# Optimization experiments

Measured on AMD Instinct MI355X. Metric: run time of the kernel, lower is better.

## Reference

```python
import jax, jax.numpy as jnp
import numpy as np

N_UNARY = 16  # unary predicate count; joined width = 2*N_UNARY + 4 = 36

# Clauses parsed from KENN strings: (literal column indices, literal signs).
# Negated literal ('n' prefix) -> sign -1, positive -> +1.
UNARY_CLAUSES = [
    ([0, 1], [-1, 1]),
    ([1, 2], [-1, 1]),
    ([2, 3, 4], [-1, 1, 1]),
    ([4, 5], [-1, 1]),
    ([6, 7, 8], [-1, 1, 1]),
    ([8, 9], [-1, 1]),
    ([10, 11, 12], [-1, 1, 1]),
    ([13, 14, 15], [-1, 1, 1]),
]
# Joined-matrix columns: [0:16]=unary(x), [16:32]=unary(y), [32:36]=binary.
BINARY_CLAUSES = [
    ([0, 32, 16], [-1, -1, 1]),
    ([1, 33, 17], [-1, -1, 1]),
    ([2, 34, 18], [-1, -1, 1]),
    ([3, 35, 19], [-1, -1, 1]),
]


def _enhance(x, clauses, weights):
    """KnowledgeEnhancer: sum over ClauseEnhancer deltas.

    Per clause: gather literal columns, flip negated literals, softmax over
    literals (t-conorm boost), scale by clause weight, flip signs back, and
    scatter-add into the full predicate width.
    """
    delta = jnp.zeros_like(x)
    for i, (idx, sgn) in enumerate(clauses):
        idx_a = jnp.asarray(idx)
        sgn_a = jnp.asarray(sgn, x.dtype)
        sel = x[:, idx_a] * sgn_a                      # [N, k] signed literal preactivations
        contrib = weights[i] * sgn_a * jax.nn.softmax(sel, axis=1)
        delta = delta.at[:, idx_a].add(contrib)
    return delta


def setup_inputs() -> dict:
    key = jax.random.key(0)
    k1, k2, k3, k4 = jax.random.split(key, 4)
    n_nodes, n_edges = 100000, 2000000
    unary = jax.random.normal(k1, (n_nodes, N_UNARY), dtype=jnp.float32)
    binary = jax.random.normal(k2, (n_edges, 4), dtype=jnp.float32)
    index1 = jax.random.randint(k3, (n_edges,), 0, n_nodes)
    index2 = jax.random.randint(k4, (n_edges,), 0, n_nodes)
    # learnable clause weights ('_' weights), initial_clause_weight = 0.5
    unary_weights = jnp.full((len(UNARY_CLAUSES),), 0.5, dtype=jnp.float32)
    binary_weights = jnp.full((len(BINARY_CLAUSES),), 0.5, dtype=jnp.float32)
    return {
        "unary": unary,
        "binary": binary,
        "index1": index1,
        "index2": index2,
        "unary_weights": unary_weights,
        "binary_weights": binary_weights,
    }


def reference(unary, binary, index1, index2, unary_weights, binary_weights):
    # unary knowledge enhancement (residual)
    u = unary + _enhance(unary, UNARY_CLAUSES, unary_weights)
    # Join: gather endpoint unary rows, concat with binary -> [E, 2*n_unary + n_binary]
    joined = jnp.concatenate([u[index1], u[index2], binary], axis=1)
    # binary knowledge enhancement on the joined matrix
    deltas = _enhance(joined, BINARY_CLAUSES, binary_weights)
    # GroupBy: split deltas and scatter-reduce unary parts back to nodes
    du1 = deltas[:, :N_UNARY]
    du2 = deltas[:, N_UNARY:2 * N_UNARY]
    db = deltas[:, 2 * N_UNARY:]
    up = u.at[index1].add(du1).at[index2].add(du2)
    bp = binary + db
    # activation = identity (default lambda x: x)
    return up, bp
```

## Files before the change

kernel.cpp:

```cpp
#include <hip/hip_runtime.h>
#include <hip/hip_bf16.h>


#define NRANGE 13
#define RBITS  13
#define RSIZE  8192
#define NSLICE 16
#define EPB    1024
#define SEGCAP 1024
#define FXP_SCALE 2048.0f
#define FXP_INV   (1.0f / 2048.0f)

__device__ __forceinline__ void sm2(float xi, float xj, float w,
                                    float& di, float& dj) {
    float na = -xi, b = xj;
    float m  = fmaxf(na, b);
    float e0 = __expf(na - m), e1 = __expf(b - m);
    float inv = w / (e0 + e1);
    di -= e0 * inv;
    dj += e1 * inv;
}

__device__ __forceinline__ void sm3(float xi, float xj, float xk, float w,
                                    float& di, float& dj, float& dk) {
    float na = -xi, b = xj, c = xk;
    float m  = fmaxf(fmaxf(na, b), c);
    float e0 = __expf(na - m), e1 = __expf(b - m), e2 = __expf(c - m);
    float inv = w / (e0 + e1 + e2);
    di -= e0 * inv;
    dj += e1 * inv;
    dk += e2 * inv;
}

__global__ void unary_kernel(const float* __restrict__ x_in,
                             const float* __restrict__ uw,
                             float* __restrict__ up,
                             float4* __restrict__ u4,
                             int n_nodes) {
    int n = blockIdx.x * blockDim.x + threadIdx.x;
    if (n >= n_nodes) return;

    const float4* xr = (const float4*)(x_in + (size_t)n * 16);
    float4 r0 = xr[0], r1 = xr[1], r2 = xr[2], r3 = xr[3];
    float x[16] = {r0.x, r0.y, r0.z, r0.w,
                   r1.x, r1.y, r1.z, r1.w,
                   r2.x, r2.y, r2.z, r2.w,
                   r3.x, r3.y, r3.z, r3.w};
    float d[16];
#pragma unroll
    for (int i = 0; i < 16; ++i) d[i] = 0.0f;

    sm2(x[0],  x[1],          uw[0], d[0],  d[1]);
    sm2(x[1],  x[2],          uw[1], d[1],  d[2]);
    sm3(x[2],  x[3],  x[4],   uw[2], d[2],  d[3],  d[4]);
    sm2(x[4],  x[5],          uw[3], d[4],  d[5]);
    sm3(x[6],  x[7],  x[8],   uw[4], d[6],  d[7],  d[8]);
    sm2(x[8],  x[9],          uw[5], d[8],  d[9]);
    sm3(x[10], x[11], x[12],  uw[6], d[10], d[11], d[12]);
    sm3(x[13], x[14], x[15],  uw[7], d[13], d[14], d[15]);

    float4* w_up = (float4*)(up + (size_t)n * 16);
    float4 v0 = make_float4(x[0] + d[0], x[1] + d[1], x[2] + d[2], x[3] + d[3]);
    w_up[0] = v0;
#pragma unroll
    for (int i = 1; i < 4; ++i)
        w_up[i] = make_float4(x[4*i]   + d[4*i],   x[4*i+1] + d[4*i+1],
                              x[4*i+2] + d[4*i+2], x[4*i+3] + d[4*i+3]);
    u4[n] = v0;
}


__global__ __launch_bounds__(512)
void edge_compute_kernel(const float4* __restrict__ u4,
                         const float4* __restrict__ binary,
                         const int* __restrict__ idx1,
                         const int* __restrict__ idx2,
                         const float* __restrict__ bw,
                         unsigned long long* __restrict__ recs,
                         unsigned* __restrict__ cnts,
                         unsigned* __restrict__ offs,
                         float4* __restrict__ bp,
                         int n_edges) {
    __shared__ unsigned cnt[2][NRANGE];
    __shared__ unsigned off[2][NRANGE];
    int tid = threadIdx.x;
    if (tid < 2 * NRANGE) ((unsigned*)cnt)[tid] = 0;
    __syncthreads();

    float w[4] = {bw[0], bw[1], bw[2], bw[3]};

    int e[2]; bool valid[2];
    int i1[2], i2[2], r1[2], r2[2];
    unsigned rank1[2], rank2[2];
    unsigned long long q1[2], q2[2];
    float4 b4[2], a4[2], c4[2], dbv4[2];

#pragma unroll
    for (int k = 0; k < 2; ++k) {
        e[k] = blockIdx.x * EPB + k * 512 + tid;
        valid[k] = e[k] < n_edges;
        int ec = valid[k] ? e[k] : 0;
        i1[k] = idx1[ec];
        i2[k] = idx2[ec];
    }
#pragma unroll
    for (int k = 0; k < 2; ++k) {
        a4[k] = u4[i1[k]];
        c4[k] = u4[i2[k]];
        b4[k] = binary[valid[k] ? e[k] : 0];
    }

#pragma unroll
    for (int k = 0; k < 2; ++k) {
        float a[4]  = {a4[k].x, a4[k].y, a4[k].z, a4[k].w};
        float bb[4] = {b4[k].x, b4[k].y, b4[k].z, b4[k].w};
        float c[4]  = {c4[k].x, c4[k].y, c4[k].z, c4[k].w};
        unsigned p1[4], p2[4];
        float dbv[4];
#pragma unroll
        for (int i = 0; i < 4; ++i) {
            float na = -a[i], nb = -bb[i], cc = c[i];
            float m  = fmaxf(fmaxf(na, nb), cc);
            float e0 = __expf(na - m), e1 = __expf(nb - m), e2 = __expf(cc - m);
            float inv = w[i] / (e0 + e1 + e2);
            p1[i]  = __float2uint_rn(e0 * inv * FXP_SCALE);
            p2[i]  = __float2uint_rn(e2 * inv * FXP_SCALE);
            dbv[i] = bb[i] - e1 * inv;
        }
        q1[k] = (unsigned long long)(unsigned)(i1[k] & (RSIZE - 1))
              | ((unsigned long long)p1[0] << 13) | ((unsigned long long)p1[1] << 25)
              | ((unsigned long long)p1[2] << 37) | ((unsigned long long)p1[3] << 49);
        q2[k] = (unsigned long long)(unsigned)(i2[k] & (RSIZE - 1))
              | ((unsigned long long)p2[0] << 13) | ((unsigned long long)p2[1] << 25)
              | ((unsigned long long)p2[2] << 37) | ((unsigned long long)p2[3] << 49);
        dbv4[k] = make_float4(dbv[0], dbv[1], dbv[2], dbv[3]);
        r1[k] = i1[k] >> RBITS;
        r2[k] = i2[k] >> RBITS;
        if (valid[k]) {
            rank1[k] = atomicAdd(&cnt[0][r1[k]], 1u);
            rank2[k] = atomicAdd(&cnt[1][r2[k]], 1u);
        }
    }
    __syncthreads();
    if (tid < 2) {
        unsigned acc = 0;
#pragma unroll
        for (int r = 0; r < NRANGE; ++r) { off[tid][r] = acc; acc += cnt[tid][r]; }
    }
    __syncthreads();
    if (tid < 2 * NRANGE) {
        cnts[(size_t)blockIdx.x * 2 * NRANGE + tid] = ((unsigned*)cnt)[tid];
        offs[(size_t)blockIdx.x * 2 * NRANGE + tid] = ((unsigned*)off)[tid];
    }
    size_t segN = (size_t)blockIdx.x * 2 * SEGCAP;
#pragma unroll
    for (int k = 0; k < 2; ++k) {
        if (!valid[k]) continue;
        recs[segN          + off[0][r1[k]] + rank1[k]] = q1[k];
        recs[segN + SEGCAP + off[1][r2[k]] + rank2[k]] = q2[k];
        bp[e[k]] = dbv4[k];
    }
}

__global__ __launch_bounds__(1024)
void bin_kernel(const unsigned long long* __restrict__ recs,
                const unsigned* __restrict__ cnts,
                const unsigned* __restrict__ offs,
                unsigned long long* __restrict__ partials,
                int nblk) {
    __shared__ unsigned long long table[RSIZE];
    unsigned b    = blockIdx.x;
    unsigned s    = b % NSLICE;
    unsigned rr   = (b / NSLICE) % NRANGE;
    unsigned side = b / (NSLICE * NRANGE);

    for (int i = threadIdx.x; i < RSIZE; i += 1024) table[i] = 0ull;
    __syncthreads();

    unsigned bpg = ((unsigned)nblk + NSLICE - 1) / NSLICE;
    unsigned b0 = s * bpg;
    unsigned b1 = b0 + bpg;
    if (b1 > (unsigned)nblk) b1 = (unsigned)nblk;

    unsigned wid  = threadIdx.x >> 6;
    unsigned lane = threadIdx.x & 63;
    unsigned eb = b0 + wid;
    unsigned c_cur = 0, o_cur = 0;
    if (eb < b1) {
        unsigned base = (eb * 2u + side) * NRANGE + rr;
        c_cur = cnts[base];
        o_cur = offs[base];
    }
    while (eb < b1) {
        unsigned eb_n = eb + 16;
        unsigned c_n = 0, o_n = 0;
        if (eb_n < b1) {
            unsigned base_n = (eb_n * 2u + side) * NRANGE + rr;
            c_n = cnts[base_n];
            o_n = offs[base_n];
        }
        const unsigned long long* seg =
            recs + ((size_t)eb * 2 + side) * SEGCAP + o_cur;
        unsigned i = lane;
        for (; i + 64 < c_cur; i += 128) {
            unsigned long long ra = seg[i];
            unsigned long long rb = seg[i + 64];
            unsigned long long va =  ((ra >> 13) & 0xFFFull)
                                  | (((ra >> 25) & 0xFFFull) << 16)
                                  | (((ra >> 37) & 0xFFFull) << 32)
                                  | (((ra >> 49) & 0xFFFull) << 48);
            unsigned long long vb =  ((rb >> 13) & 0xFFFull)
                                  | (((rb >> 25) & 0xFFFull) << 16)
                                  | (((rb >> 37) & 0xFFFull) << 32)
                                  | (((rb >> 49) & 0xFFFull) << 48);
            atomicAdd(&table[(unsigned)ra & (RSIZE - 1)], va);
            atomicAdd(&table[(unsigned)rb & (RSIZE - 1)], vb);
        }
        if (i < c_cur) {
            unsigned long long ra = seg[i];
            unsigned long long va =  ((ra >> 13) & 0xFFFull)
                                  | (((ra >> 25) & 0xFFFull) << 16)
                                  | (((ra >> 37) & 0xFFFull) << 32)
                                  | (((ra >> 49) & 0xFFFull) << 48);
            atomicAdd(&table[(unsigned)ra & (RSIZE - 1)], va);
        }
        eb = eb_n;
        c_cur = c_n;
        o_cur = o_n;
    }
    __syncthreads();

    unsigned long long* dst = partials + (size_t)b * RSIZE;
    for (int i2 = threadIdx.x; i2 < RSIZE; i2 += 1024) dst[i2] = table[i2];
}

__global__ void merge_bin_kernel(const unsigned long long* __restrict__ partials,
                                 float* __restrict__ up, int n_nodes) {
    int n = blockIdx.x * blockDim.x + threadIdx.x;
    if (n >= n_nodes) return;
    unsigned rr = (unsigned)n >> RBITS;
    unsigned i  = (unsigned)n & (RSIZE - 1);

    const unsigned long long* pn =
        partials + ((size_t)(0 * NRANGE + rr) * NSLICE) * RSIZE + i;
    const unsigned long long* pp =
        partials + ((size_t)(1 * NRANGE + rr) * NSLICE) * RSIZE + i;
    unsigned long long qn = 0, qp = 0;
#pragma unroll
    for (int sl = 0; sl < NSLICE; ++sl) {
        qn += pn[(size_t)sl * RSIZE];
        qp += pp[(size_t)sl * RSIZE];
    }

    float4* dst = (float4*)(up + (size_t)n * 16);
    float4 cur = dst[0];
    float d0 = ((float)(unsigned)( qp        & 0xFFFF) -
                (float)(unsigned)( qn        & 0xFFFF)) * FXP_INV;
    float d1 = ((float)(unsigned)((qp >> 16) & 0xFFFF) -
                (float)(unsigned)((qn >> 16) & 0xFFFF)) * FXP_INV;
    float d2 = ((float)(unsigned)((qp >> 32) & 0xFFFF) -
                (float)(unsigned)((qn >> 32) & 0xFFFF)) * FXP_INV;
    float d3 = ((float)(unsigned)((qp >> 48) & 0xFFFF) -
                (float)(unsigned)((qn >> 48) & 0xFFFF)) * FXP_INV;
    dst[0] = make_float4(cur.x + d0, cur.y + d1, cur.z + d2, cur.w + d3);
}


__global__ void edge_atomic_kernel(const float* __restrict__ u,
                                   const float4* __restrict__ binary,
                                   const int* __restrict__ idx1,
                                   const int* __restrict__ idx2,
                                   const float* __restrict__ bw,
                                   unsigned long long* __restrict__ neg,
                                   unsigned long long* __restrict__ pos,
                                   float4* __restrict__ bp,
                                   int n_edges) {
    int e = blockIdx.x * blockDim.x + threadIdx.x;
    if (e >= n_edges) return;
    int n1 = idx1[e], n2 = idx2[e];
    float4 b4 = binary[e];
    float4 a4 = *(const float4*)(u + (size_t)n1 * 16);
    float4 c4 = *(const float4*)(u + (size_t)n2 * 16);
    float a[4]  = {a4.x, a4.y, a4.z, a4.w};
    float bb[4] = {b4.x, b4.y, b4.z, b4.w};
    float c[4]  = {c4.x, c4.y, c4.z, c4.w};
    unsigned long long q1 = 0, q2 = 0;
    float dbv[4];
#pragma unroll
    for (int i = 0; i < 4; ++i) {
        float na = -a[i], nb = -bb[i], cc = c[i];
        float m  = fmaxf(fmaxf(na, nb), cc);
        float e0 = __expf(na - m), e1 = __expf(nb - m), e2 = __expf(cc - m);
        float inv = bw[i] / (e0 + e1 + e2);
        q1 |= (unsigned long long)__float2uint_rn(e0 * inv * FXP_SCALE) << (16 * i);
        q2 |= (unsigned long long)__float2uint_rn(e2 * inv * FXP_SCALE) << (16 * i);
        dbv[i] = bb[i] - e1 * inv;
    }
    atomicAdd(&neg[n1], q1);
    atomicAdd(&pos[n2], q2);
    bp[e] = make_float4(dbv[0], dbv[1], dbv[2], dbv[3]);
}

__global__ void merge_atomic_kernel(const unsigned long long* __restrict__ neg,
                                    const unsigned long long* __restrict__ pos,
                                    float* __restrict__ up, int n_nodes) {
    int n = blockIdx.x * blockDim.x + threadIdx.x;
    if (n >= n_nodes) return;
    unsigned long long qn = neg[n], qp = pos[n];
    float4* dst = (float4*)(up + (size_t)n * 16);
    float4 cur = dst[0];
    float d0 = ((float)(unsigned)( qp        & 0xFFFF) -
                (float)(unsigned)( qn        & 0xFFFF)) * FXP_INV;
    float d1 = ((float)(unsigned)((qp >> 16) & 0xFFFF) -
                (float)(unsigned)((qn >> 16) & 0xFFFF)) * FXP_INV;
    float d2 = ((float)(unsigned)((qp >> 32) & 0xFFFF) -
                (float)(unsigned)((qn >> 32) & 0xFFFF)) * FXP_INV;
    float d3 = ((float)(unsigned)((qp >> 48) & 0xFFFF) -
                (float)(unsigned)((qn >> 48) & 0xFFFF)) * FXP_INV;
    dst[0] = make_float4(cur.x + d0, cur.y + d1, cur.z + d2, cur.w + d3);
}

extern "C" void kernel_launch(void* const* d_in, const int* in_sizes, int n_in,
                              void* d_out, int out_size, void* d_ws, size_t ws_size,
                              hipStream_t stream) {
    const float* unary   = (const float*)d_in[0];
    const float* binary  = (const float*)d_in[1];
    const int*   index1  = (const int*)d_in[2];
    const int*   index2  = (const int*)d_in[3];
    const float* uw      = (const float*)d_in[4];
    const float* bw      = (const float*)d_in[5];

    int n_nodes = in_sizes[0] / 16;
    int n_edges = in_sizes[2];

    float* out = (float*)d_out;
    float* up  = out;
    float* bp  = out + (size_t)n_nodes * 16;

    int nblk = (n_edges + EPB - 1) / EPB;

    size_t rec_bytes  = (size_t)nblk * 2 * SEGCAP * 8;
    size_t part_bytes = (size_t)2 * NRANGE * NSLICE * RSIZE * 8;
    size_t u4_bytes   = (size_t)n_nodes * 16;
    size_t cnt_bytes  = (size_t)nblk * 2 * NRANGE * 4;
    size_t need = rec_bytes + part_bytes + u4_bytes + 2 * cnt_bytes + 256;

    if (ws_size >= need) {
        char* w = (char*)d_ws;
        unsigned long long* recs     = (unsigned long long*)w;
        unsigned long long* partials = (unsigned long long*)(w + rec_bytes);
        float4*   u4   = (float4*)(w + rec_bytes + part_bytes);
        unsigned* cnts = (unsigned*)(w + rec_bytes + part_bytes + u4_bytes);
        unsigned* offs = cnts + (size_t)nblk * 2 * NRANGE;

        unary_kernel<<<(n_nodes + 255) / 256, 256, 0, stream>>>(
            unary, uw, up, u4, n_nodes);
        edge_compute_kernel<<<nblk, 512, 0, stream>>>(
            u4, (const float4*)binary, index1, index2, bw,
            recs, cnts, offs, (float4*)bp, n_edges);
        bin_kernel<<<2 * NRANGE * NSLICE, 1024, 0, stream>>>(
            recs, cnts, offs, partials, nblk);
        merge_bin_kernel<<<(n_nodes + 255) / 256, 256, 0, stream>>>(
            partials, up, n_nodes);
    } else {
        unsigned long long* neg = (unsigned long long*)d_ws;
        unsigned long long* pos = neg + n_nodes;
        float4* u4 = (float4*)(pos + n_nodes);
        hipMemsetAsync(neg, 0, (size_t)2 * n_nodes * 8, stream);
        unary_kernel<<<(n_nodes + 255) / 256, 256, 0, stream>>>(
            unary, uw, up, u4, n_nodes);
        edge_atomic_kernel<<<(n_edges + 255) / 256, 256, 0, stream>>>(
            up, (const float4*)binary, index1, index2, bw,
            neg, pos, (float4*)bp, n_edges);
        merge_atomic_kernel<<<(n_nodes + 255) / 256, 256, 0, stream>>>(
            neg, pos, up, n_nodes);
    }
}
```

Before: 168.4 us.

## Fuse four-stage binning pipeline into one persistent cooperative kernel with grid syncs

Replaces the four separate launches (unary, edge compute, bin, merge) with a single persistent cooperative kernel that runs each phase in a grid-stride loop and separates them with grid.sync. Edge records are first staged in LDS and then written out coalesced instead of scattered to global memory, and the binary output uses nontemporal stores. Chunk size doubles to 2048 edges per block. This targets launch overhead and scattered writes, but the grid is limited to about two blocks per CU, so the bin phase's 416 work items and the edge phase run with less parallelism. It also adds grid-wide barrier costs and host-side occupancy queries on every call.

New measurement: 599.7 us. +256.2%, slower.

```diff
diff --git a/kernel.cpp b/kernel.cpp
--- a/kernel.cpp
+++ b/kernel.cpp
@@ -1,15 +1,23 @@
 #include <hip/hip_runtime.h>
-#include <hip/hip_bf16.h>
+#include <hip/hip_cooperative_groups.h>
+
+namespace cg = cooperative_groups;
 
 
 #define NRANGE 13
 #define RBITS  13
 #define RSIZE  8192
 #define NSLICE 16
-#define EPB    1024
-#define SEGCAP 1024
+#define EPB    2048
 #define FXP_SCALE 2048.0f
 #define FXP_INV   (1.0f / 2048.0f)
+
+typedef float nf4 __attribute__((ext_vector_type(4)));
+
+__device__ __forceinline__ void nt_store_f4(float4 v, float4* p) {
+    nf4 t; t.x = v.x; t.y = v.y; t.z = v.z; t.w = v.w;
+    __builtin_nontemporal_store(t, (nf4*)p);
+}
 
 __device__ __forceinline__ void sm2(float xi, float xj, float w,
                                     float& di, float& dj) {
@@ -32,6 +40,247 @@
     dk += e2 * inv;
 }
 
+
+__global__ __launch_bounds__(1024, 8)
+void fused_kernel(const float* __restrict__ x_in,
+                  const float4* __restrict__ binary,
+                  const int* __restrict__ idx1,
+                  const int* __restrict__ idx2,
+                  const float* __restrict__ uw,
+                  const float* __restrict__ bw,
+                  float* __restrict__ up,
+                  float4* __restrict__ bp,
+                  float4* __restrict__ u4,
+                  unsigned long long* __restrict__ recs,
+                  unsigned* __restrict__ cnts,
+                  unsigned* __restrict__ offs,
+                  unsigned long long* __restrict__ partials,
+                  int n_nodes, int n_edges, int nchunk) {
+    __shared__ union SH {
+        struct {
+            unsigned cnt[2][NRANGE];
+            unsigned off[2][NRANGE];
+            unsigned long long stage[2][EPB];
+        } e;
+        unsigned long long table[RSIZE];
+    } sh;
+
+    cg::grid_group grid = cg::this_grid();
+    const int tid     = threadIdx.x;
+    const int nthread = gridDim.x * 1024;
+
+    for (int n = blockIdx.x * 1024 + tid; n < n_nodes; n += nthread) {
+        const float4* xr = (const float4*)(x_in + (size_t)n * 16);
+        float4 r0 = xr[0], r1 = xr[1], r2 = xr[2], r3 = xr[3];
+        float x[16] = {r0.x, r0.y, r0.z, r0.w, r1.x, r1.y, r1.z, r1.w,
+                       r2.x, r2.y, r2.z, r2.w, r3.x, r3.y, r3.z, r3.w};
+        float d[16];
+#pragma unroll
+        for (int i = 0; i < 16; ++i) d[i] = 0.0f;
+        sm2(x[0],  x[1],          uw[0], d[0],  d[1]);
+        sm2(x[1],  x[2],          uw[1], d[1],  d[2]);
+        sm3(x[2],  x[3],  x[4],   uw[2], d[2],  d[3],  d[4]);
+        sm2(x[4],  x[5],          uw[3], d[4],  d[5]);
+        sm3(x[6],  x[7],  x[8],   uw[4], d[6],  d[7],  d[8]);
+        sm2(x[8],  x[9],          uw[5], d[8],  d[9]);
+        sm3(x[10], x[11], x[12],  uw[6], d[10], d[11], d[12]);
+        sm3(x[13], x[14], x[15],  uw[7], d[13], d[14], d[15]);
+        float4* w_up = (float4*)(up + (size_t)n * 16);
+        float4 v0 = make_float4(x[0]+d[0], x[1]+d[1], x[2]+d[2], x[3]+d[3]);
+        w_up[0] = v0;
+#pragma unroll
+        for (int i = 1; i < 4; ++i)
+            w_up[i] = make_float4(x[4*i]+d[4*i],     x[4*i+1]+d[4*i+1],
+                                  x[4*i+2]+d[4*i+2], x[4*i+3]+d[4*i+3]);
+        u4[n] = v0;
+    }
+    __threadfence();
+    grid.sync();
+
+    {
+        float w[4] = {bw[0], bw[1], bw[2], bw[3]};
+        for (int chunk = blockIdx.x; chunk < nchunk; chunk += gridDim.x) {
+            if (tid < 2 * NRANGE) ((unsigned*)sh.e.cnt)[tid] = 0;
+            __syncthreads();
+
+            int e[2]; bool valid[2];
+            int i1[2], i2[2], r1[2], r2[2];
+            unsigned rank1[2], rank2[2];
+            unsigned long long q1[2], q2[2];
+            float4 b4[2], a4[2], c4[2], dbv4[2];
+
+#pragma unroll
+            for (int k = 0; k < 2; ++k) {
+                e[k] = chunk * EPB + k * 1024 + tid;
+                valid[k] = e[k] < n_edges;
+                int ec = valid[k] ? e[k] : 0;
+                i1[k] = idx1[ec];
+                i2[k] = idx2[ec];
+            }
+#pragma unroll
+            for (int k = 0; k < 2; ++k) {
+                a4[k] = u4[i1[k]];
+                c4[k] = u4[i2[k]];
+                b4[k] = binary[valid[k] ? e[k] : 0];
+            }
+#pragma unroll
+            for (int k = 0; k < 2; ++k) {
+                float a[4]  = {a4[k].x, a4[k].y, a4[k].z, a4[k].w};
+                float bb[4] = {b4[k].x, b4[k].y, b4[k].z, b4[k].w};
+                float c[4]  = {c4[k].x, c4[k].y, c4[k].z, c4[k].w};
+                unsigned p1[4], p2[4];
+                float dbv[4];
+#pragma unroll
+                for (int i = 0; i < 4; ++i) {
+                    float na = -a[i], nb = -bb[i], cc = c[i];
+                    float m  = fmaxf(fmaxf(na, nb), cc);
+                    float e0 = __expf(na-m), e1 = __expf(nb-m), e2 = __expf(cc-m);
+                    float inv = w[i] / (e0 + e1 + e2);
+                    p1[i]  = __float2uint_rn(e0 * inv * FXP_SCALE);
+                    p2[i]  = __float2uint_rn(e2 * inv * FXP_SCALE);
+                    dbv[i] = bb[i] - e1 * inv;
+                }
+                q1[k] = (unsigned long long)(unsigned)(i1[k] & (RSIZE-1))
+                      | ((unsigned long long)p1[0] << 13) | ((unsigned long long)p1[1] << 25)
+                      | ((unsigned long long)p1[2] << 37) | ((unsigned long long)p1[3] << 49);
+                q2[k] = (unsigned long long)(unsigned)(i2[k] & (RSIZE-1))
+                      | ((unsigned long long)p2[0] << 13) | ((unsigned long long)p2[1] << 25)
+                      | ((unsigned long long)p2[2] << 37) | ((unsigned long long)p2[3] << 49);
+                dbv4[k] = make_float4(dbv[0], dbv[1], dbv[2], dbv[3]);
+                r1[k] = i1[k] >> RBITS;
+                r2[k] = i2[k] >> RBITS;
+                if (valid[k]) {
+                    rank1[k] = atomicAdd(&sh.e.cnt[0][r1[k]], 1u);
+                    rank2[k] = atomicAdd(&sh.e.cnt[1][r2[k]], 1u);
+                }
+            }
+            __syncthreads();
+            if (tid < 2) {
+                unsigned acc = 0;
+#pragma unroll
+                for (int r = 0; r < NRANGE; ++r) {
+                    sh.e.off[tid][r] = acc; acc += sh.e.cnt[tid][r];
+                }
+            }
+            __syncthreads();
+            if (tid < 2 * NRANGE) {
+                cnts[(size_t)chunk * 2 * NRANGE + tid] = ((unsigned*)sh.e.cnt)[tid];
+                offs[(size_t)chunk * 2 * NRANGE + tid] = ((unsigned*)sh.e.off)[tid];
+            }
+#pragma unroll
+            for (int k = 0; k < 2; ++k) {
+                if (!valid[k]) continue;
+                sh.e.stage[0][sh.e.off[0][r1[k]] + rank1[k]] = q1[k];
+                sh.e.stage[1][sh.e.off[1][r2[k]] + rank2[k]] = q2[k];
+                nt_store_f4(dbv4[k], bp + e[k]);
+            }
+            __syncthreads();
+            ulonglong2* dst = (ulonglong2*)(recs + (size_t)chunk * 2 * EPB);
+            const ulonglong2* s0 = (const ulonglong2*)sh.e.stage[0];
+            const ulonglong2* s1 = (const ulonglong2*)sh.e.stage[1];
+            dst[tid]        = s0[tid];
+            dst[1024 + tid] = s1[tid];
+        }
+    }
+    __threadfence();
+    grid.sync();
+
+    for (int b = blockIdx.x; b < 2 * NRANGE * NSLICE; b += gridDim.x) {
+        unsigned s    = (unsigned)b % NSLICE;
+        unsigned rr   = ((unsigned)b / NSLICE) % NRANGE;
+        unsigned side = (unsigned)b / (NSLICE * NRANGE);
+
+        for (int i = tid; i < RSIZE; i += 1024) sh.table[i] = 0ull;
+        __syncthreads();
+
+        unsigned bpg = ((unsigned)nchunk + NSLICE - 1) / NSLICE;
+        unsigned b0 = s * bpg;
+        unsigned b1 = b0 + bpg;
+        if (b1 > (unsigned)nchunk) b1 = (unsigned)nchunk;
+
+        unsigned wid  = (unsigned)tid >> 6;
+        unsigned lane = (unsigned)tid & 63;
+        unsigned eb = b0 + wid;
+        unsigned c_cur = 0, o_cur = 0;
+        if (eb < b1) {
+            unsigned base = (eb * 2u + side) * NRANGE + rr;
+            c_cur = cnts[base];
+            o_cur = offs[base];
+        }
+        while (eb < b1) {
+            unsigned eb_n = eb + 16;
+            unsigned c_n = 0, o_n = 0;
+            if (eb_n < b1) {
+                unsigned base_n = (eb_n * 2u + side) * NRANGE + rr;
+                c_n = cnts[base_n];
+                o_n = offs[base_n];
+            }
+            const unsigned long long* seg =
+                recs + ((size_t)eb * 2 + side) * EPB + o_cur;
+            unsigned i = lane;
+            for (; i + 64 < c_cur; i += 128) {
+                unsigned long long ra = seg[i];
+                unsigned long long rb = seg[i + 64];
+                unsigned long long va =  ((ra >> 13) & 0xFFFull)
+                                      | (((ra >> 25) & 0xFFFull) << 16)
+                                      | (((ra >> 37) & 0xFFFull) << 32)
+                                      | (((ra >> 49) & 0xFFFull) << 48);
+                unsigned long long vb =  ((rb >> 13) & 0xFFFull)
+                                      | (((rb >> 25) & 0xFFFull) << 16)
+                                      | (((rb >> 37) & 0xFFFull) << 32)
+                                      | (((rb >> 49) & 0xFFFull) << 48);
+                atomicAdd(&sh.table[(unsigned)ra & (RSIZE - 1)], va);
+                atomicAdd(&sh.table[(unsigned)rb & (RSIZE - 1)], vb);
+            }
+            if (i < c_cur) {
+                unsigned long long ra = seg[i];
+                unsigned long long va =  ((ra >> 13) & 0xFFFull)
+                                      | (((ra >> 25) & 0xFFFull) << 16)
+                                      | (((ra >> 37) & 0xFFFull) << 32)
+                                      | (((ra >> 49) & 0xFFFull) << 48);
+                atomicAdd(&sh.table[(unsigned)ra & (RSIZE - 1)], va);
+            }
+            eb = eb_n;
+            c_cur = c_n;
+            o_cur = o_n;
+        }
+        __syncthreads();
+
+        unsigned long long* dst = partials + (size_t)b * RSIZE;
+        for (int i2 = tid; i2 < RSIZE; i2 += 1024) dst[i2] = sh.table[i2];
+        __syncthreads();
+    }
+    __threadfence();
+    grid.sync();
+
+    for (int n = blockIdx.x * 1024 + tid; n < n_nodes; n += nthread) {
+        unsigned rr = (unsigned)n >> RBITS;
+        unsigned i  = (unsigned)n & (RSIZE - 1);
+        const unsigned long long* pn =
+            partials + ((size_t)(0 * NRANGE + rr) * NSLICE) * RSIZE + i;
+        const unsigned long long* pp =
+            partials + ((size_t)(1 * NRANGE + rr) * NSLICE) * RSIZE + i;
+        unsigned long long qn = 0, qp = 0;
+#pragma unroll
+        for (int sl = 0; sl < NSLICE; ++sl) {
+            qn += pn[(size_t)sl * RSIZE];
+            qp += pp[(size_t)sl * RSIZE];
+        }
+        float4* dst = (float4*)(up + (size_t)n * 16);
+        float4 cur = dst[0];
+        float d0 = ((float)(unsigned)( qp        & 0xFFFF) -
+                    (float)(unsigned)( qn        & 0xFFFF)) * FXP_INV;
+        float d1 = ((float)(unsigned)((qp >> 16) & 0xFFFF) -
+                    (float)(unsigned)((qn >> 16) & 0xFFFF)) * FXP_INV;
+        float d2 = ((float)(unsigned)((qp >> 32) & 0xFFFF) -
+                    (float)(unsigned)((qn >> 32) & 0xFFFF)) * FXP_INV;
+        float d3 = ((float)(unsigned)((qp >> 48) & 0xFFFF) -
+                    (float)(unsigned)((qn >> 48) & 0xFFFF)) * FXP_INV;
+        dst[0] = make_float4(cur.x + d0, cur.y + d1, cur.z + d2, cur.w + d3);
+    }
+}
+
+
 __global__ void unary_kernel(const float* __restrict__ x_in,
                              const float* __restrict__ uw,
                              float* __restrict__ up,
@@ -39,17 +288,13 @@
                              int n_nodes) {
     int n = blockIdx.x * blockDim.x + threadIdx.x;
     if (n >= n_nodes) return;
-
     const float4* xr = (const float4*)(x_in + (size_t)n * 16);
     float4 r0 = xr[0], r1 = xr[1], r2 = xr[2], r3 = xr[3];
-    float x[16] = {r0.x, r0.y, r0.z, r0.w,
-                   r1.x, r1.y, r1.z, r1.w,
-                   r2.x, r2.y, r2.z, r2.w,
-                   r3.x, r3.y, r3.z, r3.w};
+    float x[16] = {r0.x, r0.y, r0.z, r0.w, r1.x, r1.y, r1.z, r1.w,
+                   r2.x, r2.y, r2.z, r2.w, r3.x, r3.y, r3.z, r3.w};
     float d[16];
 #pragma unroll
     for (int i = 0; i < 16; ++i) d[i] = 0.0f;
-
     sm2(x[0],  x[1],          uw[0], d[0],  d[1]);
     sm2(x[1],  x[2],          uw[1], d[1],  d[2]);
     sm3(x[2],  x[3],  x[4],   uw[2], d[2],  d[3],  d[4]);
@@ -58,213 +303,15 @@
     sm2(x[8],  x[9],          uw[5], d[8],  d[9]);
     sm3(x[10], x[11], x[12],  uw[6], d[10], d[11], d[12]);
     sm3(x[13], x[14], x[15],  uw[7], d[13], d[14], d[15]);
-
     float4* w_up = (float4*)(up + (size_t)n * 16);
-    float4 v0 = make_float4(x[0] + d[0], x[1] + d[1], x[2] + d[2], x[3] + d[3]);
+    float4 v0 = make_float4(x[0]+d[0], x[1]+d[1], x[2]+d[2], x[3]+d[3]);
     w_up[0] = v0;
 #pragma unroll
     for (int i = 1; i < 4; ++i)
-        w_up[i] = make_float4(x[4*i]   + d[4*i],   x[4*i+1] + d[4*i+1],
-                              x[4*i+2] + d[4*i+2], x[4*i+3] + d[4*i+3]);
+        w_up[i] = make_float4(x[4*i]+d[4*i],     x[4*i+1]+d[4*i+1],
+                              x[4*i+2]+d[4*i+2], x[4*i+3]+d[4*i+3]);
     u4[n] = v0;
 }
-
-
-__global__ __launch_bounds__(512)
-void edge_compute_kernel(const float4* __restrict__ u4,
-                         const float4* __restrict__ binary,
-                         const int* __restrict__ idx1,
-                         const int* __restrict__ idx2,
-                         const float* __restrict__ bw,
-                         unsigned long long* __restrict__ recs,
-                         unsigned* __restrict__ cnts,
-                         unsigned* __restrict__ offs,
-                         float4* __restrict__ bp,
-                         int n_edges) {
-    __shared__ unsigned cnt[2][NRANGE];
-    __shared__ unsigned off[2][NRANGE];
-    int tid = threadIdx.x;
-    if (tid < 2 * NRANGE) ((unsigned*)cnt)[tid] = 0;
-    __syncthreads();
-
-    float w[4] = {bw[0], bw[1], bw[2], bw[3]};
-
-    int e[2]; bool valid[2];
-    int i1[2], i2[2], r1[2], r2[2];
-    unsigned rank1[2], rank2[2];
-    unsigned long long q1[2], q2[2];
-    float4 b4[2], a4[2], c4[2], dbv4[2];
-
-#pragma unroll
-    for (int k = 0; k < 2; ++k) {
-        e[k] = blockIdx.x * EPB + k * 512 + tid;
-        valid[k] = e[k] < n_edges;
-        int ec = valid[k] ? e[k] : 0;
-        i1[k] = idx1[ec];
-        i2[k] = idx2[ec];
-    }
-#pragma unroll
-    for (int k = 0; k < 2; ++k) {
-        a4[k] = u4[i1[k]];
-        c4[k] = u4[i2[k]];
-        b4[k] = binary[valid[k] ? e[k] : 0];
-    }
-
-#pragma unroll
-    for (int k = 0; k < 2; ++k) {
-        float a[4]  = {a4[k].x, a4[k].y, a4[k].z, a4[k].w};
-        float bb[4] = {b4[k].x, b4[k].y, b4[k].z, b4[k].w};
-        float c[4]  = {c4[k].x, c4[k].y, c4[k].z, c4[k].w};
-        unsigned p1[4], p2[4];
-        float dbv[4];
-#pragma unroll
-        for (int i = 0; i < 4; ++i) {
-            float na = -a[i], nb = -bb[i], cc = c[i];
-            float m  = fmaxf(fmaxf(na, nb), cc);
-            float e0 = __expf(na - m), e1 = __expf(nb - m), e2 = __expf(cc - m);
-            float inv = w[i] / (e0 + e1 + e2);
-            p1[i]  = __float2uint_rn(e0 * inv * FXP_SCALE);
-            p2[i]  = __float2uint_rn(e2 * inv * FXP_SCALE);
-            dbv[i] = bb[i] - e1 * inv;
-        }
-        q1[k] = (unsigned long long)(unsigned)(i1[k] & (RSIZE - 1))
-              | ((unsigned long long)p1[0] << 13) | ((unsigned long long)p1[1] << 25)
-              | ((unsigned long long)p1[2] << 37) | ((unsigned long long)p1[3] << 49);
-        q2[k] = (unsigned long long)(unsigned)(i2[k] & (RSIZE - 1))
-              | ((unsigned long long)p2[0] << 13) | ((unsigned long long)p2[1] << 25)
-              | ((unsigned long long)p2[2] << 37) | ((unsigned long long)p2[3] << 49);
-        dbv4[k] = make_float4(dbv[0], dbv[1], dbv[2], dbv[3]);
-        r1[k] = i1[k] >> RBITS;
-        r2[k] = i2[k] >> RBITS;
-        if (valid[k]) {
-            rank1[k] = atomicAdd(&cnt[0][r1[k]], 1u);
-            rank2[k] = atomicAdd(&cnt[1][r2[k]], 1u);
-        }
-    }
-    __syncthreads();
-    if (tid < 2) {
-        unsigned acc = 0;
-#pragma unroll
-        for (int r = 0; r < NRANGE; ++r) { off[tid][r] = acc; acc += cnt[tid][r]; }
-    }
-    __syncthreads();
-    if (tid < 2 * NRANGE) {
-        cnts[(size_t)blockIdx.x * 2 * NRANGE + tid] = ((unsigned*)cnt)[tid];
-        offs[(size_t)blockIdx.x * 2 * NRANGE + tid] = ((unsigned*)off)[tid];
-    }
-    size_t segN = (size_t)blockIdx.x * 2 * SEGCAP;
-#pragma unroll
-    for (int k = 0; k < 2; ++k) {
-        if (!valid[k]) continue;
-        recs[segN          + off[0][r1[k]] + rank1[k]] = q1[k];
-        recs[segN + SEGCAP + off[1][r2[k]] + rank2[k]] = q2[k];
-        bp[e[k]] = dbv4[k];
-    }
-}
-
-__global__ __launch_bounds__(1024)
-void bin_kernel(const unsigned long long* __restrict__ recs,
-                const unsigned* __restrict__ cnts,
-                const unsigned* __restrict__ offs,
-                unsigned long long* __restrict__ partials,
-                int nblk) {
-    __shared__ unsigned long long table[RSIZE];
-    unsigned b    = blockIdx.x;
-    unsigned s    = b % NSLICE;
-    unsigned rr   = (b / NSLICE) % NRANGE;
-    unsigned side = b / (NSLICE * NRANGE);
-
-    for (int i = threadIdx.x; i < RSIZE; i += 1024) table[i] = 0ull;
-    __syncthreads();
-
-    unsigned bpg = ((unsigned)nblk + NSLICE - 1) / NSLICE;
-    unsigned b0 = s * bpg;
-    unsigned b1 = b0 + bpg;
-    if (b1 > (unsigned)nblk) b1 = (unsigned)nblk;
-
-    unsigned wid  = threadIdx.x >> 6;
-    unsigned lane = threadIdx.x & 63;
-    unsigned eb = b0 + wid;
-    unsigned c_cur = 0, o_cur = 0;
-    if (eb < b1) {
-        unsigned base = (eb * 2u + side) * NRANGE + rr;
-        c_cur = cnts[base];
-        o_cur = offs[base];
-    }
-    while (eb < b1) {
-        unsigned eb_n = eb + 16;
-        unsigned c_n = 0, o_n = 0;
-        if (eb_n < b1) {
-            unsigned base_n = (eb_n * 2u + side) * NRANGE + rr;
-            c_n = cnts[base_n];
-            o_n = offs[base_n];
-        }
-        const unsigned long long* seg =
-            recs + ((size_t)eb * 2 + side) * SEGCAP + o_cur;
-        unsigned i = lane;
-        for (; i + 64 < c_cur; i += 128) {
-            unsigned long long ra = seg[i];
-            unsigned long long rb = seg[i + 64];
-            unsigned long long va =  ((ra >> 13) & 0xFFFull)
-                                  | (((ra >> 25) & 0xFFFull) << 16)
-                                  | (((ra >> 37) & 0xFFFull) << 32)
-                                  | (((ra >> 49) & 0xFFFull) << 48);
-            unsigned long long vb =  ((rb >> 13) & 0xFFFull)
-                                  | (((rb >> 25) & 0xFFFull) << 16)
-                                  | (((rb >> 37) & 0xFFFull) << 32)
-                                  | (((rb >> 49) & 0xFFFull) << 48);
-            atomicAdd(&table[(unsigned)ra & (RSIZE - 1)], va);
-            atomicAdd(&table[(unsigned)rb & (RSIZE - 1)], vb);
-        }
-        if (i < c_cur) {
-            unsigned long long ra = seg[i];
-            unsigned long long va =  ((ra >> 13) & 0xFFFull)
-                                  | (((ra >> 25) & 0xFFFull) << 16)
-                                  | (((ra >> 37) & 0xFFFull) << 32)
-                                  | (((ra >> 49) & 0xFFFull) << 48);
-            atomicAdd(&table[(unsigned)ra & (RSIZE - 1)], va);
-        }
-        eb = eb_n;
-        c_cur = c_n;
-        o_cur = o_n;
-    }
-    __syncthreads();
-
-    unsigned long long* dst = partials + (size_t)b * RSIZE;
-    for (int i2 = threadIdx.x; i2 < RSIZE; i2 += 1024) dst[i2] = table[i2];
-}
-
-__global__ void merge_bin_kernel(const unsigned long long* __restrict__ partials,
-                                 float* __restrict__ up, int n_nodes) {
-    int n = blockIdx.x * blockDim.x + threadIdx.x;
-    if (n >= n_nodes) return;
-    unsigned rr = (unsigned)n >> RBITS;
-    unsigned i  = (unsigned)n & (RSIZE - 1);
-
-    const unsigned long long* pn =
-        partials + ((size_t)(0 * NRANGE + rr) * NSLICE) * RSIZE + i;
-    const unsigned long long* pp =
-        partials + ((size_t)(1 * NRANGE + rr) * NSLICE) * RSIZE + i;
-    unsigned long long qn = 0, qp = 0;
-#pragma unroll
-    for (int sl = 0; sl < NSLICE; ++sl) {
-        qn += pn[(size_t)sl * RSIZE];
-        qp += pp[(size_t)sl * RSIZE];
-    }
-
-    float4* dst = (float4*)(up + (size_t)n * 16);
-    float4 cur = dst[0];
-    float d0 = ((float)(unsigned)( qp        & 0xFFFF) -
-                (float)(unsigned)( qn        & 0xFFFF)) * FXP_INV;
-    float d1 = ((float)(unsigned)((qp >> 16) & 0xFFFF) -
-                (float)(unsigned)((qn >> 16) & 0xFFFF)) * FXP_INV;
-    float d2 = ((float)(unsigned)((qp >> 32) & 0xFFFF) -
-                (float)(unsigned)((qn >> 32) & 0xFFFF)) * FXP_INV;
-    float d3 = ((float)(unsigned)((qp >> 48) & 0xFFFF) -
-                (float)(unsigned)((qn >> 48) & 0xFFFF)) * FXP_INV;
-    dst[0] = make_float4(cur.x + d0, cur.y + d1, cur.z + d2, cur.w + d3);
-}
-
 
 __global__ void edge_atomic_kernel(const float* __restrict__ u,
                                    const float4* __restrict__ binary,
@@ -290,7 +337,7 @@
     for (int i = 0; i < 4; ++i) {
         float na = -a[i], nb = -bb[i], cc = c[i];
         float m  = fmaxf(fmaxf(na, nb), cc);
-        float e0 = __expf(na - m), e1 = __expf(nb - m), e2 = __expf(cc - m);
+        float e0 = __expf(na-m), e1 = __expf(nb-m), e2 = __expf(cc-m);
         float inv = bw[i] / (e0 + e1 + e2);
         q1 |= (unsigned long long)__float2uint_rn(e0 * inv * FXP_SCALE) << (16 * i);
         q2 |= (unsigned long long)__float2uint_rn(e2 * inv * FXP_SCALE) << (16 * i);
@@ -337,12 +384,12 @@
     float* up  = out;
     float* bp  = out + (size_t)n_nodes * 16;
 
-    int nblk = (n_edges + EPB - 1) / EPB;
-
-    size_t rec_bytes  = (size_t)nblk * 2 * SEGCAP * 8;
+    int nchunk = (n_edges + EPB - 1) / EPB;
+
+    size_t rec_bytes  = (size_t)nchunk * 2 * EPB * 8;
     size_t part_bytes = (size_t)2 * NRANGE * NSLICE * RSIZE * 8;
     size_t u4_bytes   = (size_t)n_nodes * 16;
-    size_t cnt_bytes  = (size_t)nblk * 2 * NRANGE * 4;
+    size_t cnt_bytes  = (size_t)nchunk * 2 * NRANGE * 4;
     size_t need = rec_bytes + part_bytes + u4_bytes + 2 * cnt_bytes + 256;
 
     if (ws_size >= need) {
@@ -351,22 +398,34 @@
         unsigned long long* partials = (unsigned long long*)(w + rec_bytes);
         float4*   u4   = (float4*)(w + rec_bytes + part_bytes);
         unsigned* cnts = (unsigned*)(w + rec_bytes + part_bytes + u4_bytes);
-        unsigned* offs = cnts + (size_t)nblk * 2 * NRANGE;
-
-        unary_kernel<<<(n_nodes + 255) / 256, 256, 0, stream>>>(
-            unary, uw, up, u4, n_nodes);
-        edge_compute_kernel<<<nblk, 512, 0, stream>>>(
-            u4, (const float4*)binary, index1, index2, bw,
-            recs, cnts, offs, (float4*)bp, n_edges);
-        bin_kernel<<<2 * NRANGE * NSLICE, 1024, 0, stream>>>(
-            recs, cnts, offs, partials, nblk);
-        merge_bin_kernel<<<(n_nodes + 255) / 256, 256, 0, stream>>>(
-            partials, up, n_nodes);
+        unsigned* offs = cnts + (size_t)nchunk * 2 * NRANGE;
+
+        const float4* binary4 = (const float4*)binary;
+        float4* bp4 = (float4*)bp;
+
+        int num_cu = 256;
+        (void)hipDeviceGetAttribute(&num_cu, hipDeviceAttributeMultiprocessorCount, 0);
+        int maxblk = 2;
+        (void)hipOccupancyMaxActiveBlocksPerMultiprocessor(&maxblk, fused_kernel,
+                                                           1024, 0);
+        if (maxblk < 1) maxblk = 1;
+        if (maxblk > 2) maxblk = 2;
+        int grid = num_cu * maxblk;
+
+        void* args[] = {
+            (void*)&unary, (void*)&binary4, (void*)&index1, (void*)&index2,
+            (void*)&uw, (void*)&bw, (void*)&up, (void*)&bp4, (void*)&u4,
+            (void*)&recs, (void*)&cnts, (void*)&offs, (void*)&partials,
+            (void*)&n_nodes, (void*)&n_edges, (void*)&nchunk
+        };
+        (void)hipLaunchCooperativeKernel((const void*)fused_kernel,
+                                         dim3(grid), dim3(1024),
+                                         args, 0, stream);
     } else {
         unsigned long long* neg = (unsigned long long*)d_ws;
         unsigned long long* pos = neg + n_nodes;
         float4* u4 = (float4*)(pos + n_nodes);
-        hipMemsetAsync(neg, 0, (size_t)2 * n_nodes * 8, stream);
+        (void)hipMemsetAsync(neg, 0, (size_t)2 * n_nodes * 8, stream);
         unary_kernel<<<(n_nodes + 255) / 256, 256, 0, stream>>>(
             unary, uw, up, u4, n_nodes);
         edge_atomic_kernel<<<(n_edges + 255) / 256, 256, 0, stream>>>(
```
